# Performance work log

Measured on AMD Instinct MI355X. Metric: run time of the kernel, lower is better.

## Reference

```python
import jax, jax.numpy as jnp
import numpy as np

KH, KW = 7, 7            # extraction kernel
EH, EW = 5, 5            # effective (cropped) kernel
PAD = (KH - EH) // 2     # = 1
EPS = 1e-7


def _extract_patches(x):
    # x: [B,H,W,C] -> patches [B,Ho,Wo,KH,KW,C], stride 1, VALID padding
    B, H, Wd, C = x.shape
    Ho, Wo = H - KH + 1, Wd - KW + 1
    rows = []
    for i in range(KH):
        cols = [x[:, i:i + Ho, j:j + Wo, :] for j in range(KW)]
        rows.append(jnp.stack(cols, axis=3))          # [B,Ho,Wo,KW,C]
    return jnp.stack(rows, axis=3)                     # [B,Ho,Wo,KH,KW,C]


def _rotate_bilinear(patches, angles):
    # patches: [N,KH,KW,C]; angles: [N]. Mirrors tf.contrib.image
    # angles_to_projective_transforms + transform(BILINEAR, fill=0).
    # Note: the layer's det(matrix)==0 NEAREST fallback never fires (det==1).
    N = patches.shape[0]
    c, s = jnp.cos(angles), jnp.sin(angles)
    Wm1, Hm1 = jnp.float32(KW - 1), jnp.float32(KH - 1)
    xo = (Wm1 - (c * Wm1 - s * Hm1)) * 0.5
    yo = (Hm1 - (s * Wm1 + c * Hm1)) * 0.5
    scale = jnp.float32(1.0 + EPS)   # transforms /= transforms[:,8:9]+1e-7
    a0, a1, a2 = c / scale, -s / scale, xo / scale
    a3, a4, a5 = s / scale, c / scale, yo / scale
    yg, xg = jnp.meshgrid(jnp.arange(KH, dtype=jnp.float32),
                          jnp.arange(KW, dtype=jnp.float32), indexing='ij')
    x_in = a0[:, None, None] * xg + a1[:, None, None] * yg + a2[:, None, None]
    y_in = a3[:, None, None] * xg + a4[:, None, None] * yg + a5[:, None, None]
    x0f = jnp.floor(x_in); y0f = jnp.floor(y_in)
    wx1 = x_in - x0f; wx0 = 1.0 - wx1
    wy1 = y_in - y0f; wy0 = 1.0 - wy1
    x0 = x0f.astype(jnp.int32); x1 = x0 + 1
    y0 = y0f.astype(jnp.int32); y1 = y0 + 1
    nidx = jnp.arange(N)[:, None, None]

    def corner(yi, xi, w):
        valid = ((xi >= 0) & (xi < KW) & (yi >= 0) & (yi < KH)).astype(patches.dtype)
        v = patches[nidx, jnp.clip(yi, 0, KH - 1), jnp.clip(xi, 0, KW - 1)]
        return (w * valid)[..., None] * v

    return (corner(y0, x0, wy0 * wx0) + corner(y0, x1, wy0 * wx1) +
            corner(y1, x0, wy1 * wx0) + corner(y1, x1, wy1 * wx1))


def reference(x, W, b):
    B, H, Wd, C = x.shape
    patches = _extract_patches(x)                      # [B,Ho,Wo,KH,KW,C]
    _, Ho, Wo = patches.shape[:3]
    intensity = jnp.sum(patches, axis=-1)              # [B,Ho,Wo,KH,KW]
    row_idx = jnp.repeat(jnp.arange(KH, dtype=jnp.float32), KW)   # rowMulti
    col_idx = jnp.tile(jnp.arange(KW, dtype=jnp.float32), KH)     # colMulti
    flat = intensity.reshape(-1, KH * KW)              # [N, KH*KW]
    denom = jnp.sum(flat, -1) + EPS
    cr = jnp.sum(flat * row_idx, -1) / denom - (KH - 1) / 2.0
    cc = jnp.sum(flat * col_idx, -1) / denom - (KW - 1) / 2.0
    angle = jnp.arctan2(cr, cc + EPS)                  # [N]
    patches_n = patches.reshape(-1, KH, KW, C)         # [N,KH,KW,C]
    rot = _rotate_bilinear(patches_n, angle)
    rot = rot[:, PAD:PAD + EH, PAD:PAD + EW, :]        # crop to effective
    rot = rot.reshape(B, Ho, Wo, EH * EW * C)
    w_flat = W.reshape(W.shape[0], -1)                 # [F, EH*EW*C]
    out = jnp.einsum('bhwk,fk->bhwf', rot, w_flat) + b
    return out


def setup_inputs() -> dict:
    key = jax.random.key(0)
    kx, kw, _ = jax.random.split(key, 3)
    x = jax.random.normal(kx, (8, 64, 64, 32), dtype=jnp.float32)
    W = jax.random.normal(kw, (64, EH, EW, 32), dtype=jnp.float32) * 0.05
    b = jnp.zeros((64,), dtype=jnp.float32)
    return {"x": x, "W": W, "b": b}
```

## Files before the change

kernel.cpp:

```cpp
#include <hip/hip_runtime.h>
#include <hip/hip_bf16.h>

#define EPSF 1e-7f
#define B_ 8
#define H_ 64
#define W_ 64
#define C_ 32
#define HO 58
#define WO 58
#define NF 64
#define KDIM 800

#define XBS 40
#define RS  808

typedef __bf16 v8bf __attribute__((ext_vector_type(8)));
typedef float  v4f  __attribute__((ext_vector_type(4)));
typedef float  v2f  __attribute__((ext_vector_type(2)));

__global__ void k_wpack(const float* __restrict__ W, __bf16* __restrict__ Wp) {
    int t = blockIdx.x*256 + threadIdx.x;
    int j = t & 7; int lane = (t >> 3) & 63; int rest = t >> 9;
    int kb = rest % 25; int nt = rest / 25;
    int f = nt*16 + (lane & 15);
    int k = kb*32 + (lane >> 4)*8 + j;
    Wp[t] = (__bf16)W[f*KDIM + k];
}

__global__ __launch_bounds__(256, 4)
void k_main(const float* __restrict__ x, const v8bf* __restrict__ Wp,
            const float* __restrict__ bias, float* __restrict__ out) {
    __shared__ __bf16 xtb[8][22][XBS];
    __shared__ __bf16 rot[16][RS];
    __shared__ float  Srow[8][22];

    int tid = threadIdx.x;
    int wv = tid >> 6, lane = tid & 63;
    int m = lane & 15, q = lane >> 4;

    int L = blockIdx.x + 4*(blockIdx.y + 29*blockIdx.z);
    int newL = (L & 7)*116 + (L >> 3);
    int b   = newL / 116;
    int rem = newL - b*116;
    int hog = rem >> 2;
    int wt  = rem & 3;
    int ho0 = hog*2;

    int wo0 = wt*16;
    int npx = WO - wo0; if (npx > 16) npx = 16;
    int ncols = npx + 6;

    float bv = bias[wv*16 + m];

    if (tid < 8*ncols) {
        int r, c;
        if (ncols == 22) { r = tid/22; c = tid - r*22; }
        else             { r = tid >> 4; c = tid & 15; }
        const float* src = x + (size_t)((b*H_ + ho0 + r)*W_ + wo0 + c)*C_;
        float4 vq[8];
#pragma unroll
        for (int qq = 0; qq < 8; qq++) vq[qq] = *(const float4*)(src + qq*4);
        float s = 0.f;
#pragma unroll
        for (int qq = 0; qq < 8; qq++) s += vq[qq].x + vq[qq].y + vq[qq].z + vq[qq].w;
        Srow[r][c] = s;
#pragma unroll
        for (int h8 = 0; h8 < 4; h8++) {
            v8bf o;
            o[0]=(__bf16)vq[h8*2].x;   o[1]=(__bf16)vq[h8*2].y;
            o[2]=(__bf16)vq[h8*2].z;   o[3]=(__bf16)vq[h8*2].w;
            o[4]=(__bf16)vq[h8*2+1].x; o[5]=(__bf16)vq[h8*2+1].y;
            o[6]=(__bf16)vq[h8*2+1].z; o[7]=(__bf16)vq[h8*2+1].w;
            *(v8bf*)&xtb[r][c][h8*8] = o;
        }
    }
    __syncthreads();

    int slot = lane & 7;
    int g = (lane >> 3) & 7;
    int myT = g & 1;
    int myC = wv*4 + (g >> 1);
    float den = 0.f, crn = 0.f, ccn = 0.f;
    if (slot < 7) {
#pragma unroll
        for (int j = 0; j < 7; j++) {
            float v = Srow[myT + slot][myC + j];
            den += v; crn += v*(float)slot; ccn += v*(float)j;
        }
    }
#pragma unroll
    for (int msk = 1; msk <= 4; msk <<= 1) {
        den += __shfl_xor(den, msk);
        crn += __shfl_xor(crn, msk);
        ccn += __shfl_xor(ccn, msk);
    }
    float pc, ps, pxo, pyo;
    {
        float dt = den + EPSF;
        float cr = crn/dt - 3.0f;
        float cx = ccn/dt - 3.0f + EPSF;
        float r2 = cr*cr + cx*cx;
        float inv = r2 > 0.f ? rsqrtf(r2) : 0.f;
        float c = r2 > 0.f ? cx*inv : 1.0f;
        float s = cr*inv;
        const float scale = 1.0f + EPSF;
        pc  = c/scale; ps = s/scale;
        pxo = (6.0f - (c*6.0f - s*6.0f))*0.5f/scale;
        pyo = (6.0f - (s*6.0f + c*6.0f))*0.5f/scale;
    }
    float pc2  = __shfl_xor(pc, 8),  ps2  = __shfl_xor(ps, 8);
    float pxo2 = __shfl_xor(pxo, 8), pyo2 = __shfl_xor(pyo, 8);

    auto do_rot = [&](int t, int pos, float c_, float s_, float xo_, float yo_) {
        int pxl = wv*4 + q;
        int py = pos/5; int yy = py + 1; int xx = pos - py*5 + 1;
        float xin = c_*(float)xx - s_*(float)yy + xo_;
        float yin = s_*(float)xx + c_*(float)yy + yo_;
        float x0f = floorf(xin), y0f = floorf(yin);
        float wx1 = xin - x0f, wx0 = 1.0f - wx1;
        float wy1 = yin - y0f, wy0 = 1.0f - wy1;
        int ix0 = (int)x0f, iy0 = (int)y0f;
        int ix1 = ix0 + 1,  iy1 = iy0 + 1;

        const __bf16* bp[4]; float wgt[4];
        auto mkcorner = [&](int yi, int xi, float w, int idx) {
            bool valid = (xi >= 0) & (xi < 7) & (yi >= 0) & (yi < 7);
            int cy = yi < 0 ? 0 : (yi > 6 ? 6 : yi);
            int cx2 = xi < 0 ? 0 : (xi > 6 ? 6 : xi);
            bp[idx]  = &xtb[t + cy][pxl + cx2][0];
            wgt[idx] = valid ? w : 0.0f;
        };
        mkcorner(iy0, ix0, wy0*wx0, 0);
        mkcorner(iy0, ix1, wy0*wx1, 1);
        mkcorner(iy1, ix0, wy1*wx0, 2);
        mkcorner(iy1, ix1, wy1*wx1, 3);

        v2f acc[16];
#pragma unroll
        for (int i = 0; i < 16; i++) acc[i] = (v2f){0.f, 0.f};
#pragma unroll
        for (int cn = 0; cn < 4; cn++) {
            const __bf16* src = bp[cn];
            v2f wq2 = (v2f){wgt[cn], wgt[cn]};
#pragma unroll
            for (int q8 = 0; q8 < 4; q8++) {
                union { v8bf v; unsigned u[4]; } uv;
                uv.v = *(const v8bf*)(src + q8*8);
#pragma unroll
                for (int d = 0; d < 4; d++) {
                    v2f val = (v2f){ __uint_as_float(uv.u[d] << 16),
                                     __uint_as_float(uv.u[d] & 0xffff0000u) };
                    acc[q8*4 + d] += wq2 * val;
                }
            }
        }
#pragma unroll
        for (int q8 = 0; q8 < 4; q8++) {
            v8bf o;
#pragma unroll
            for (int d = 0; d < 4; d++) {
                o[2*d]   = (__bf16)acc[q8*4 + d].x;
                o[2*d+1] = (__bf16)acc[q8*4 + d].y;
            }
            *(v8bf*)&rot[pxl][pos*32 + q8*8] = o;
        }
    };

    float c0 = (myT == 0) ? pc : pc2,   s0 = (myT == 0) ? ps : ps2;
    float xo0 = (myT == 0) ? pxo : pxo2, yo0 = (myT == 0) ? pyo : pyo2;
    float c1 = (myT == 1) ? pc : pc2,   s1 = (myT == 1) ? ps : ps2;
    float xo1 = (myT == 1) ? pxo : pxo2, yo1 = (myT == 1) ? pyo : pyo2;

    const v8bf* wp = Wp + (size_t)wv*25*64 + lane;
    int f = wv*16 + m;
    int pixbase0 = (b*HO + ho0)*WO + wo0;

#pragma unroll
    for (int t = 0; t < 2; t++) {
        float tc  = t ? c1  : c0,  ts  = t ? s1  : s0;
        float txo = t ? xo1 : xo0, tyo = t ? yo1 : yo0;
        if (t) __syncthreads();
#pragma unroll
        for (int rnd = 0; rnd < 2; rnd++) {
            int pos = m + 16*rnd;
            if (pos < 25) do_rot(t, pos, tc, ts, txo, tyo);
        }
        v8bf bfA[13];
#pragma unroll
        for (int kb = 0; kb < 13; kb++) bfA[kb] = wp[kb*64];
        __syncthreads();

        v8bf bfB[12];
#pragma unroll
        for (int kb = 0; kb < 12; kb++) bfB[kb] = wp[(13 + kb)*64];

        v4f acc0 = {0.f, 0.f, 0.f, 0.f};
        v4f acc1 = {0.f, 0.f, 0.f, 0.f};
#pragma unroll
        for (int kb = 0; kb < 13; kb++) {
            v8bf a = *(const v8bf*)&rot[m][kb*32 + q*8];
            if (kb & 1) acc1 = __builtin_amdgcn_mfma_f32_16x16x32_bf16(a, bfA[kb], acc1, 0, 0, 0);
            else        acc0 = __builtin_amdgcn_mfma_f32_16x16x32_bf16(a, bfA[kb], acc0, 0, 0, 0);
        }
#pragma unroll
        for (int kb = 0; kb < 12; kb++) {
            v8bf a = *(const v8bf*)&rot[m][(13 + kb)*32 + q*8];
            if (kb & 1) acc1 = __builtin_amdgcn_mfma_f32_16x16x32_bf16(a, bfB[kb], acc1, 0, 0, 0);
            else        acc0 = __builtin_amdgcn_mfma_f32_16x16x32_bf16(a, bfB[kb], acc0, 0, 0, 0);
        }

        int pixbase = pixbase0 + t*WO;
#pragma unroll
        for (int r = 0; r < 4; r++) {
            int px = q*4 + r;
            if (px < npx) out[(size_t)(pixbase + px)*NF + f] = acc0[r] + acc1[r] + bv;
        }
    }
}

extern "C" void kernel_launch(void* const* d_in, const int* in_sizes, int n_in,
                              void* d_out, int out_size, void* d_ws, size_t ws_size,
                              hipStream_t stream) {
    const float* x    = (const float*)d_in[0];
    const float* W    = (const float*)d_in[1];
    const float* bias = (const float*)d_in[2];
    float* out = (float*)d_out;
    __bf16* Wp = (__bf16*)d_ws;

    k_wpack<<<dim3(200), 256, 0, stream>>>(W, Wp);
    k_main<<<dim3(4, 29, B_), 256, 0, stream>>>(x, (const v8bf*)Wp, bias, out);
}
```

Measured before the change: 76.36 us.

## Fuse bilinear rotation into MFMA A-operand, drop rot smem, 4 rows per block

The rotated patch tile is no longer staged in shared memory. Each lane computes its bilinear-rotated 8-channel A fragment directly in registers and feeds it straight into four MFMAs, one per 16-filter group. Each block now covers 4 output rows by 16 columns, with one wave per row, and the orientation parameters are computed once per pixel into shared memory. This removes the rot buffer, its write/read round trip and the extra barriers. In exchange every wave loads all 64 filters' weights from global memory per k-block, and the grid shrinks to 480 blocks with lower occupancy bounds.

```diff
diff --git a/kernel.cpp b/kernel.cpp
--- a/kernel.cpp
+++ b/kernel.cpp
@@ -12,7 +12,6 @@
 #define KDIM 800
 
 #define XBS 40
-#define RS  808
 
 typedef __bf16 v8bf __attribute__((ext_vector_type(8)));
 typedef float  v4f  __attribute__((ext_vector_type(4)));
@@ -27,36 +26,31 @@
     Wp[t] = (__bf16)W[f*KDIM + k];
 }
 
-__global__ __launch_bounds__(256, 4)
+__global__ __launch_bounds__(256, 3)
 void k_main(const float* __restrict__ x, const v8bf* __restrict__ Wp,
             const float* __restrict__ bias, float* __restrict__ out) {
-    __shared__ __bf16 xtb[8][22][XBS];
-    __shared__ __bf16 rot[16][RS];
-    __shared__ float  Srow[8][22];
+    __shared__ __bf16 xtb[10][22][XBS];
+    __shared__ float  Srow[10][22];
+    __shared__ float4 pars[64];
 
     int tid = threadIdx.x;
     int wv = tid >> 6, lane = tid & 63;
     int m = lane & 15, q = lane >> 4;
 
-    int L = blockIdx.x + 4*(blockIdx.y + 29*blockIdx.z);
-    int newL = (L & 7)*116 + (L >> 3);
-    int b   = newL / 116;
-    int rem = newL - b*116;
-    int hog = rem >> 2;
-    int wt  = rem & 3;
-    int ho0 = hog*2;
+    int L = blockIdx.x + 4*(blockIdx.y + 15*blockIdx.z);
+    int newL = (L & 7)*60 + (L >> 3);
+    int b   = newL / 60;
+    int rem = newL - b*60;
+    int rg  = rem >> 2;
+    int cg  = rem & 3;
+    int ho0 = rg*4, wo0 = cg*16;
+    int npx = WO - wo0; if (npx > 16) npx = 16;
 
-    int wo0 = wt*16;
-    int npx = WO - wo0; if (npx > 16) npx = 16;
-    int ncols = npx + 6;
-
-    float bv = bias[wv*16 + m];
-
-    if (tid < 8*ncols) {
-        int r, c;
-        if (ncols == 22) { r = tid/22; c = tid - r*22; }
-        else             { r = tid >> 4; c = tid & 15; }
-        const float* src = x + (size_t)((b*H_ + ho0 + r)*W_ + wo0 + c)*C_;
+    if (tid < 220) {
+        int r = tid / 22, c = tid - r*22;
+        int xr = ho0 + r; if (xr > H_-1) xr = H_-1;
+        int xc = wo0 + c; if (xc > W_-1) xc = W_-1;
+        const float* src = x + (size_t)((b*H_ + xr)*W_ + xc)*C_;
         float4 vq[8];
 #pragma unroll
         for (int qq = 0; qq < 8; qq++) vq[qq] = *(const float4*)(src + qq*4);
@@ -76,144 +70,115 @@
     }
     __syncthreads();
 
-    int slot = lane & 7;
-    int g = (lane >> 3) & 7;
-    int myT = g & 1;
-    int myC = wv*4 + (g >> 1);
-    float den = 0.f, crn = 0.f, ccn = 0.f;
-    if (slot < 7) {
+    if (tid < 64) {
+        int r0 = tid >> 4, c0 = tid & 15;
+        float den = 0.f, crn = 0.f, ccn = 0.f;
 #pragma unroll
-        for (int j = 0; j < 7; j++) {
-            float v = Srow[myT + slot][myC + j];
-            den += v; crn += v*(float)slot; ccn += v*(float)j;
-        }
-    }
+        for (int i = 0; i < 7; i++)
 #pragma unroll
-    for (int msk = 1; msk <= 4; msk <<= 1) {
-        den += __shfl_xor(den, msk);
-        crn += __shfl_xor(crn, msk);
-        ccn += __shfl_xor(ccn, msk);
-    }
-    float pc, ps, pxo, pyo;
-    {
+            for (int j = 0; j < 7; j++) {
+                float v = Srow[r0 + i][c0 + j];
+                den += v; crn += v*(float)i; ccn += v*(float)j;
+            }
         float dt = den + EPSF;
         float cr = crn/dt - 3.0f;
         float cx = ccn/dt - 3.0f + EPSF;
         float r2 = cr*cr + cx*cx;
         float inv = r2 > 0.f ? rsqrtf(r2) : 0.f;
-        float c = r2 > 0.f ? cx*inv : 1.0f;
-        float s = cr*inv;
+        float c_ = r2 > 0.f ? cx*inv : 1.0f;
+        float s_ = cr*inv;
         const float scale = 1.0f + EPSF;
-        pc  = c/scale; ps = s/scale;
-        pxo = (6.0f - (c*6.0f - s*6.0f))*0.5f/scale;
-        pyo = (6.0f - (s*6.0f + c*6.0f))*0.5f/scale;
+        float pc  = c_/scale, ps = s_/scale;
+        float pxo = (6.0f - (c_*6.0f - s_*6.0f))*0.5f/scale;
+        float pyo = (6.0f - (s_*6.0f + c_*6.0f))*0.5f/scale;
+        pars[tid] = make_float4(pc, ps, pxo, pyo);
     }
-    float pc2  = __shfl_xor(pc, 8),  ps2  = __shfl_xor(ps, 8);
-    float pxo2 = __shfl_xor(pxo, 8), pyo2 = __shfl_xor(pyo, 8);
+    __syncthreads();
 
-    auto do_rot = [&](int t, int pos, float c_, float s_, float xo_, float yo_) {
-        int pxl = wv*4 + q;
-        int py = pos/5; int yy = py + 1; int xx = pos - py*5 + 1;
-        float xin = c_*(float)xx - s_*(float)yy + xo_;
-        float yin = s_*(float)xx + c_*(float)yy + yo_;
-        float x0f = floorf(xin), y0f = floorf(yin);
-        float wx1 = xin - x0f, wx0 = 1.0f - wx1;
-        float wy1 = yin - y0f, wy0 = 1.0f - wy1;
-        int ix0 = (int)x0f, iy0 = (int)y0f;
-        int ix1 = ix0 + 1,  iy1 = iy0 + 1;
+    float4 pp = pars[(wv << 4) | m];
+    float pc = pp.x, ps = pp.y, pxo = pp.z, pyo = pp.w;
 
-        const __bf16* bp[4]; float wgt[4];
-        auto mkcorner = [&](int yi, int xi, float w, int idx) {
-            bool valid = (xi >= 0) & (xi < 7) & (yi >= 0) & (yi < 7);
-            int cy = yi < 0 ? 0 : (yi > 6 ? 6 : yi);
-            int cx2 = xi < 0 ? 0 : (xi > 6 ? 6 : xi);
-            bp[idx]  = &xtb[t + cy][pxl + cx2][0];
-            wgt[idx] = valid ? w : 0.0f;
-        };
-        mkcorner(iy0, ix0, wy0*wx0, 0);
-        mkcorner(iy0, ix1, wy0*wx1, 1);
-        mkcorner(iy1, ix0, wy1*wx0, 2);
-        mkcorner(iy1, ix1, wy1*wx1, 3);
+    float bv[4];
+#pragma unroll
+    for (int nt = 0; nt < 4; nt++) bv[nt] = bias[nt*16 + m];
 
-        v2f acc[16];
+    const v8bf* wp = Wp + lane;
+    const __bf16* patch = &xtb[wv][m][q*8];
+
+    v4f acc0 = {0.f,0.f,0.f,0.f}, acc1 = {0.f,0.f,0.f,0.f};
+    v4f acc2 = {0.f,0.f,0.f,0.f}, acc3 = {0.f,0.f,0.f,0.f};
+
+#pragma unroll 1
+    for (int py = 0; py < 5; py++) {
+        float yy = (float)(py + 1);
 #pragma unroll
-        for (int i = 0; i < 16; i++) acc[i] = (v2f){0.f, 0.f};
+        for (int pxx = 0; pxx < 5; pxx++) {
+            int kb = py*5 + pxx;
+            float xx = (float)(pxx + 1);
+
+            v8bf wf0 = wp[(0*25 + kb)*64];
+            v8bf wf1 = wp[(1*25 + kb)*64];
+            v8bf wf2 = wp[(2*25 + kb)*64];
+            v8bf wf3 = wp[(3*25 + kb)*64];
+
+            float xin = pc*xx - ps*yy + pxo;
+            float yin = ps*xx + pc*yy + pyo;
+            float x0f = floorf(xin), y0f = floorf(yin);
+            float wx1 = xin - x0f, wx0 = 1.0f - wx1;
+            float wy1 = yin - y0f, wy0 = 1.0f - wy1;
+            int ix0 = (int)x0f, iy0 = (int)y0f;
+            int ix1 = ix0 + 1,  iy1 = iy0 + 1;
+
+            v2f a8[4];
 #pragma unroll
-        for (int cn = 0; cn < 4; cn++) {
-            const __bf16* src = bp[cn];
-            v2f wq2 = (v2f){wgt[cn], wgt[cn]};
-#pragma unroll
-            for (int q8 = 0; q8 < 4; q8++) {
+            for (int d = 0; d < 4; d++) a8[d] = (v2f){0.f, 0.f};
+
+            auto corner = [&](int yi, int xi, float wgt) {
+                bool valid = (xi >= 0) & (xi < 7) & (yi >= 0) & (yi < 7);
+                int cy  = yi < 0 ? 0 : (yi > 6 ? 6 : yi);
+                int cx2 = xi < 0 ? 0 : (xi > 6 ? 6 : xi);
+                float wq = valid ? wgt : 0.0f;
                 union { v8bf v; unsigned u[4]; } uv;
-                uv.v = *(const v8bf*)(src + q8*8);
+                uv.v = *(const v8bf*)(patch + (cy*22 + cx2)*XBS);
+                v2f w2 = (v2f){wq, wq};
 #pragma unroll
                 for (int d = 0; d < 4; d++) {
                     v2f val = (v2f){ __uint_as_float(uv.u[d] << 16),
                                      __uint_as_float(uv.u[d] & 0xffff0000u) };
-                    acc[q8*4 + d] += wq2 * val;
+                    a8[d] += w2 * val;
                 }
-            }
-        }
-#pragma unroll
-        for (int q8 = 0; q8 < 4; q8++) {
-            v8bf o;
+            };
+            corner(iy0, ix0, wy0*wx0);
+            corner(iy0, ix1, wy0*wx1);
+            corner(iy1, ix0, wy1*wx0);
+            corner(iy1, ix1, wy1*wx1);
+
+            v8bf af;
 #pragma unroll
             for (int d = 0; d < 4; d++) {
-                o[2*d]   = (__bf16)acc[q8*4 + d].x;
-                o[2*d+1] = (__bf16)acc[q8*4 + d].y;
+                af[2*d]   = (__bf16)a8[d].x;
+                af[2*d+1] = (__bf16)a8[d].y;
             }
-            *(v8bf*)&rot[pxl][pos*32 + q8*8] = o;
+            acc0 = __builtin_amdgcn_mfma_f32_16x16x32_bf16(af, wf0, acc0, 0, 0, 0);
+            acc1 = __builtin_amdgcn_mfma_f32_16x16x32_bf16(af, wf1, acc1, 0, 0, 0);
+            acc2 = __builtin_amdgcn_mfma_f32_16x16x32_bf16(af, wf2, acc2, 0, 0, 0);
+            acc3 = __builtin_amdgcn_mfma_f32_16x16x32_bf16(af, wf3, acc3, 0, 0, 0);
         }
-    };
+    }
 
-    float c0 = (myT == 0) ? pc : pc2,   s0 = (myT == 0) ? ps : ps2;
-    float xo0 = (myT == 0) ? pxo : pxo2, yo0 = (myT == 0) ? pyo : pyo2;
-    float c1 = (myT == 1) ? pc : pc2,   s1 = (myT == 1) ? ps : ps2;
-    float xo1 = (myT == 1) ? pxo : pxo2, yo1 = (myT == 1) ? pyo : pyo2;
-
-    const v8bf* wp = Wp + (size_t)wv*25*64 + lane;
-    int f = wv*16 + m;
-    int pixbase0 = (b*HO + ho0)*WO + wo0;
-
-#pragma unroll
-    for (int t = 0; t < 2; t++) {
-        float tc  = t ? c1  : c0,  ts  = t ? s1  : s0;
-        float txo = t ? xo1 : xo0, tyo = t ? yo1 : yo0;
-        if (t) __syncthreads();
-#pragma unroll
-        for (int rnd = 0; rnd < 2; rnd++) {
-            int pos = m + 16*rnd;
-            if (pos < 25) do_rot(t, pos, tc, ts, txo, tyo);
-        }
-        v8bf bfA[13];
-#pragma unroll
-        for (int kb = 0; kb < 13; kb++) bfA[kb] = wp[kb*64];
-        __syncthreads();
-
-        v8bf bfB[12];
-#pragma unroll
-        for (int kb = 0; kb < 12; kb++) bfB[kb] = wp[(13 + kb)*64];
-
-        v4f acc0 = {0.f, 0.f, 0.f, 0.f};
-        v4f acc1 = {0.f, 0.f, 0.f, 0.f};
-#pragma unroll
-        for (int kb = 0; kb < 13; kb++) {
-            v8bf a = *(const v8bf*)&rot[m][kb*32 + q*8];
-            if (kb & 1) acc1 = __builtin_amdgcn_mfma_f32_16x16x32_bf16(a, bfA[kb], acc1, 0, 0, 0);
-            else        acc0 = __builtin_amdgcn_mfma_f32_16x16x32_bf16(a, bfA[kb], acc0, 0, 0, 0);
-        }
-#pragma unroll
-        for (int kb = 0; kb < 12; kb++) {
-            v8bf a = *(const v8bf*)&rot[m][(13 + kb)*32 + q*8];
-            if (kb & 1) acc1 = __builtin_amdgcn_mfma_f32_16x16x32_bf16(a, bfB[kb], acc1, 0, 0, 0);
-            else        acc0 = __builtin_amdgcn_mfma_f32_16x16x32_bf16(a, bfB[kb], acc0, 0, 0, 0);
-        }
-
-        int pixbase = pixbase0 + t*WO;
+    int ho = ho0 + wv;
+    if (ho < HO) {
+        size_t rowbase = (size_t)(b*HO + ho)*WO + wo0;
 #pragma unroll
         for (int r = 0; r < 4; r++) {
             int px = q*4 + r;
-            if (px < npx) out[(size_t)(pixbase + px)*NF + f] = acc0[r] + acc1[r] + bv;
+            if (px < npx) {
+                float* op = out + (rowbase + px)*NF + m;
+                op[0]  = acc0[r] + bv[0];
+                op[16] = acc1[r] + bv[1];
+                op[32] = acc2[r] + bv[2];
+                op[48] = acc3[r] + bv[3];
+            }
         }
     }
 }
@@ -228,5 +193,5 @@
     __bf16* Wp = (__bf16*)d_ws;
 
     k_wpack<<<dim3(200), 256, 0, stream>>>(W, Wp);
-    k_main<<<dim3(4, 29, B_), 256, 0, stream>>>(x, (const v8bf*)Wp, bias, out);
+    k_main<<<dim3(4, 15, 8), 256, 0, stream>>>(x, (const v8bf*)Wp, bias, out);
 }
```

Result: slower. 79.57 us (+4.2%).
